# Performance work log

Hardware: AMD Instinct MI355X
Metric: run time of the kernel (lower is better)

Reference implementation:

```python
import jax, jax.numpy as jnp
import numpy as np

N_NODES = 100000
N_HEDGES = 200000
N_INC = 1000000
N_GRAPHS = 256
H = 64        # h_dim
HE = 35       # hedge_fea_dim
HOUT = 128    # hout_dim
NL = 3        # n_layers
EPS = 1e-5


def _segment_mean(vals, idx, num_segments):
    s = jax.ops.segment_sum(vals, idx, num_segments=num_segments)
    cnt = jax.ops.segment_sum(jnp.ones((vals.shape[0],), vals.dtype), idx,
                              num_segments=num_segments)
    return s / jnp.maximum(cnt, 1.0)[:, None]


def _bn(z, g, b):
    # training-mode BatchNorm1d: batch stats, biased variance
    m = jnp.mean(z, axis=0)
    v = jnp.var(z, axis=0)
    return (z - m) * jax.lax.rsqrt(v + EPS) * g + b


def setup_inputs() -> dict:
    key = jax.random.key(0)
    ks = jax.random.split(key, 32)
    inp = {
        "x": jax.random.normal(ks[0], (N_NODES, 92), jnp.float32),
        "node_idx": jax.random.randint(ks[1], (N_INC,), 0, N_NODES),
        "hedge_idx": jax.random.randint(ks[2], (N_INC,), 0, N_HEDGES),
        "hedge_attr": jax.random.normal(ks[3], (N_HEDGES, HE), jnp.float32),
        "batch": jnp.sort(jax.random.randint(ks[4], (N_NODES,), 0, N_GRAPHS)),
    }
    s = 0.05
    cat = H + HE  # 99
    inp["embed_w"] = jax.random.normal(ks[5], (92, H), jnp.float32) * s
    inp["embed_b"] = jnp.zeros((H,), jnp.float32)
    inp["f1_w"] = jax.random.normal(ks[6], (NL, cat, HE), jnp.float32) * s
    inp["f1_b"] = jnp.zeros((NL, HE), jnp.float32)
    inp["c1_w"] = jax.random.normal(ks[7], (NL, cat, HE), jnp.float32) * s
    inp["c1_b"] = jnp.zeros((NL, HE), jnp.float32)
    inp["f2_w"] = jax.random.normal(ks[8], (NL, cat, H), jnp.float32) * s
    inp["f2_b"] = jnp.zeros((NL, H), jnp.float32)
    inp["c2_w"] = jax.random.normal(ks[9], (NL, cat, H), jnp.float32) * s
    inp["c2_b"] = jnp.zeros((NL, H), jnp.float32)
    inp["bnf_g"] = jnp.ones((NL, HE), jnp.float32)
    inp["bnf_b"] = jnp.zeros((NL, HE), jnp.float32)
    inp["bnc_g"] = jnp.ones((NL, HE), jnp.float32)
    inp["bnc_b"] = jnp.zeros((NL, HE), jnp.float32)
    inp["bno_g"] = jnp.ones((NL, H), jnp.float32)
    inp["bno_b"] = jnp.zeros((NL, H), jnp.float32)
    inp["l2_w"] = jax.random.normal(ks[10], (H, HOUT), jnp.float32) * s
    inp["l2_b"] = jnp.zeros((HOUT,), jnp.float32)
    inp["out_w"] = jax.random.normal(ks[11], (HOUT, 1), jnp.float32) * s
    inp["out_b"] = jnp.zeros((1,), jnp.float32)
    return inp


def reference(x, node_idx, hedge_idx, hedge_attr, batch,
              embed_w, embed_b, f1_w, f1_b, c1_w, c1_b,
              f2_w, f2_b, c2_w, c2_b,
              bnf_g, bnf_b, bnc_g, bnc_b, bno_g, bno_b,
              l2_w, l2_b, out_w, out_b):
    sp = jax.nn.softplus
    x = x @ embed_w + embed_b  # [N, H]
    for i in range(NL):
        # gather node feats per incidence, mean over each hyperedge
        hx = _segment_mean(x[node_idx], hedge_idx, N_HEDGES)       # [NH, H]
        msg = jnp.concatenate([hx, hedge_attr], axis=1)            # [NH, H+HE]
        z_f = _bn(msg @ f1_w[i] + f1_b[i], bnf_g[i], bnf_b[i])
        z_c = _bn(msg @ c1_w[i] + c1_b[i], bnc_g[i], bnc_b[i])
        hedge_attr = jax.nn.sigmoid(z_f) * sp(z_c)                 # [NH, HE]
        z = jnp.concatenate([x[node_idx], hedge_attr[hedge_idx]], axis=-1)  # [E, H+HE]
        o = jax.nn.sigmoid(z @ f2_w[i] + f2_b[i]) * sp(z @ c2_w[i] + c2_b[i])  # [E, H]
        o = _segment_mean(o, node_idx, N_NODES)                    # [N, H]
        o = _bn(o, bno_g[i], bno_b[i])
        x = sp(o + x)
    pooled = _segment_mean(x, batch, N_GRAPHS)                     # [G, H]
    h = sp(pooled @ l2_w + l2_b)                                   # [G, HOUT]
    return h @ out_w + out_b                                       # [G, 1]
```

## Files before the change

kernel.cpp:

```cpp
#include <hip/hip_runtime.h>
#include <math.h>

#define N_NODES 100000
#define N_HEDGES 200000
#define N_INC 1000000
#define N_GRAPHS 256
#define HD 64
#define HE 35
#define CAT 99
#define EPSB 1e-5f

typedef __attribute__((ext_vector_type(8))) short short8;
typedef __attribute__((ext_vector_type(4))) float f32x4;

__device__ __forceinline__ float sp_f(float x) {
  return fmaxf(x, 0.f) + __logf(1.f + __expf(-fabsf(x)));
}
__device__ __forceinline__ float sig_f(float x) {
  return __builtin_amdgcn_rcpf(1.f + __expf(-x));
}
__device__ __forceinline__ unsigned bfr(float x) {
  unsigned u = __float_as_uint(x);
  return (u + 0x7fffu + ((u >> 16) & 1u)) >> 16;
}
__device__ __forceinline__ unsigned pk2(float lo, float hi) {
  return bfr(lo) | (bfr(hi) << 16);
}
__device__ __forceinline__ float blo(unsigned v) { return __uint_as_float(v << 16); }
__device__ __forceinline__ float bhi(unsigned v) {
  return __uint_as_float(v & 0xffff0000u);
}
__device__ __forceinline__ float bf2f(unsigned short s) {
  return __uint_as_float(((unsigned)s) << 16);
}

__global__ __launch_bounds__(256) void k_hist(const int* __restrict__ nidx,
                                              const int* __restrict__ hidx,
                                              int* __restrict__ degN,
                                              int* __restrict__ degH,
                                              int* __restrict__ rankN,
                                              int* __restrict__ rankH) {
  int e = blockIdx.x * 256 + threadIdx.x;
  if (e >= N_INC) return;
  rankH[e] = atomicAdd(&degH[hidx[e]], 1);
  rankN[e] = atomicAdd(&degN[nidx[e]], 1);
}

#define CHB ((N_HEDGES + 255) / 256)
#define CNB ((N_NODES + 255) / 256)

__global__ __launch_bounds__(256) void k_bsum(const int* __restrict__ degH,
                                              const int* __restrict__ degN,
                                              int* __restrict__ bsum) {
  __shared__ int s[256];
  int b = blockIdx.x, t = threadIdx.x;
  const int* deg;
  int n, i;
  if (b < CHB) {
    deg = degH; n = N_HEDGES; i = b * 256 + t;
  } else {
    deg = degN; n = N_NODES; i = (b - CHB) * 256 + t;
  }
  s[t] = (i < n) ? deg[i] : 0;
  __syncthreads();
  for (int st = 128; st > 0; st >>= 1) {
    if (t < st) s[t] += s[t + st];
    __syncthreads();
  }
  if (t == 0) bsum[b] = s[0];
}

__global__ __launch_bounds__(64) void k_bscan(int* __restrict__ bsum) {
  int seg0 = (blockIdx.x == 0) ? 0 : CHB;
  int segn = (blockIdx.x == 0) ? CHB : CNB;
  int lane = threadIdx.x;
  int carry = 0;
  for (int base = 0; base < segn; base += 64) {
    int i = base + lane;
    int orig = (i < segn) ? bsum[seg0 + i] : 0;
    int v = orig;
    for (int st = 1; st < 64; st <<= 1) {
      int u = __shfl_up(v, st);
      if (lane >= st) v += u;
    }
    int total = __shfl(v, 63);
    if (i < segn) bsum[seg0 + i] = carry + (v - orig);
    carry += total;
  }
}

__global__ __launch_bounds__(256) void k_alloc2(const int* __restrict__ degH,
                                                const int* __restrict__ degN,
                                                const int* __restrict__ bsum,
                                                int* __restrict__ offH,
                                                int* __restrict__ offN,
                                                float* __restrict__ invdH) {
  __shared__ int s[256];
  int b = blockIdx.x, t = threadIdx.x;
  const int* deg;
  int* off;
  int n, i;
  bool isH = (b < CHB);
  if (isH) {
    deg = degH; off = offH; n = N_HEDGES; i = b * 256 + t;
  } else {
    deg = degN; off = offN; n = N_NODES; i = (b - CHB) * 256 + t;
  }
  int d = (i < n) ? deg[i] : 0;
  s[t] = d;
  __syncthreads();
  for (int st = 1; st < 256; st <<= 1) {
    int u = 0;
    if (t >= st) u = s[t - st];
    __syncthreads();
    if (t >= st) s[t] += u;
    __syncthreads();
  }
  if (i < n) {
    off[i] = s[t] - d + bsum[b];
    if (isH) invdH[i] = 1.f / (float)max(d, 1);
  }
}

__global__ __launch_bounds__(256) void k_fill(const int* __restrict__ nidx,
                                              const int* __restrict__ hidx,
                                              const int* __restrict__ rankH,
                                              const int* __restrict__ rankN,
                                              const int* __restrict__ offH,
                                              const int* __restrict__ offN,
                                              int* __restrict__ permHn,
                                              int* __restrict__ permNh) {
  int e = blockIdx.x * 256 + threadIdx.x;
  if (e >= N_INC) return;
  int nd = nidx[e], hg = hidx[e];
  permHn[offH[hg] + rankH[e]] = nd;
  permNh[offN[nd] + rankN[e]] = hg;
}

__global__ __launch_bounds__(64) void k_wpack(const float* __restrict__ f1w,
                                              const float* __restrict__ c1w,
                                              uint4* __restrict__ wpk) {
  int b = blockIdx.x;
  int layer = b / 20, rem = b % 20, ct = rem / 4, ks = rem % 4;
  int lane = threadIdx.x;
  int col = ct * 16 + (lane & 15);
  int k0 = ks * 32 + (lane >> 4) * 8;
  const float* wf = f1w + layer * CAT * HE;
  const float* wc = c1w + layer * CAT * HE;
  unsigned v[4];
#pragma unroll
  for (int p = 0; p < 4; ++p) {
    float lo = 0.f, hi = 0.f;
    int ka = k0 + p * 2, kb = ka + 1;
    if (ka < 99) {
      if (col < 35) lo = wf[ka * 35 + col];
      else if (col >= 36 && col < 71) lo = wc[ka * 35 + (col - 36)];
    }
    if (kb < 99) {
      if (col < 35) hi = wf[kb * 35 + col];
      else if (col >= 36 && col < 71) hi = wc[kb * 35 + (col - 36)];
    }
    v[p] = pk2(lo, hi);
  }
  uint4 o;
  o.x = v[0]; o.y = v[1]; o.z = v[2]; o.w = v[3];
  wpk[b * 64 + lane] = o;
}

__global__ __launch_bounds__(256) void k_cvt_ha(const float* __restrict__ src,
                                                unsigned short* __restrict__ dst,
                                                int n) {
  int t = blockIdx.x * 256 + threadIdx.x;
  if (t < n) dst[t] = (unsigned short)bfr(src[t]);
}

__global__ __launch_bounds__(256) void k_embed(const float* __restrict__ x,
                                               const float* __restrict__ w,
                                               const float* __restrict__ b,
                                               unsigned short* __restrict__ outb) {
  __shared__ float ws[92 * 64];
  __shared__ float rs[16][93];
  int tid = threadIdx.x;
  for (int i = tid; i < 92 * 64; i += 256) ws[i] = w[i];
  int r0 = blockIdx.x * 16;
  for (int i = tid; i < 16 * 92; i += 256) {
    int r = i / 92, k = i - r * 92;
    rs[r][k] = x[(r0 + r) * 92 + k];
  }
  __syncthreads();
  int h = tid & 63;
  float bias = b[h];
  for (int rr = tid >> 6; rr < 16; rr += 4) {
    float acc = bias;
    for (int k = 0; k < 92; ++k) acc += rs[rr][k] * ws[k * 64 + h];
    outb[(r0 + rr) * 64 + h] = (unsigned short)bfr(acc);
  }
}

#define GR 64
__global__ __launch_bounds__(256) void k_hedge_gemm(
    const unsigned short* __restrict__ xb, const int* __restrict__ permHn,
    const int* __restrict__ offH, const int* __restrict__ degH,
    const float* __restrict__ invdH, const unsigned short* __restrict__ hab,
    const uint4* __restrict__ wpk, unsigned short* __restrict__ z,
    float* __restrict__ stats) {
  __shared__ unsigned short msg[GR * 128];
  __shared__ float ps[160];
  int tid = threadIdx.x;
  int w = tid >> 6, lane = tid & 63;
  int r0 = blockIdx.x * GR;
  if (tid < 160) ps[tid] = 0.f;

  short8 bfg[5][4];
#pragma unroll
  for (int ct = 0; ct < 5; ++ct)
#pragma unroll
    for (int ks = 0; ks < 4; ++ks)
      bfg[ct][ks] = __builtin_bit_cast(short8, wpk[(ct * 4 + ks) * 64 + lane]);

  char* mb = (char*)msg;
  for (int r = 0; r < 16; ++r) {
    int rloc = w * 16 + r;
    int row = r0 + rloc;
    float acc = 0.f;
    unsigned short hv = 0, mv = 0;
    if (row < N_HEDGES) {
      int o = offH[row], d = degH[row];
      int k = 0;
      for (; k + 4 <= d; k += 4) {
        int n0 = permHn[o + k], n1 = permHn[o + k + 1];
        int n2 = permHn[o + k + 2], n3 = permHn[o + k + 3];
        acc += (bf2f(xb[(size_t)n0 * 64 + lane]) + bf2f(xb[(size_t)n1 * 64 + lane])) +
               (bf2f(xb[(size_t)n2 * 64 + lane]) + bf2f(xb[(size_t)n3 * 64 + lane]));
      }
      for (; k < d; ++k) acc += bf2f(xb[(size_t)permHn[o + k] * 64 + lane]);
      mv = (unsigned short)bfr(acc * invdH[row]);
      if (lane < 35) hv = hab[(size_t)row * 35 + lane];
    }
    int swz = (rloc & 7) << 4;
    *(unsigned short*)(mb + ((rloc * 256 + lane * 2) ^ swz)) = mv;
    *(unsigned short*)(mb + ((rloc * 256 + 128 + lane * 2) ^ swz)) = hv;
  }
  __syncthreads();

  {
    int rloc = w * 16 + (lane & 15);
    short8 a[4];
#pragma unroll
    for (int ks = 0; ks < 4; ++ks) {
      int byte = rloc * 256 + (ks * 32 + (lane >> 4) * 8) * 2;
      a[ks] = *(const short8*)(mb + (byte ^ ((rloc & 7) << 4)));
    }
#pragma unroll
    for (int ct = 0; ct < 5; ++ct) {
      f32x4 acc = {0.f, 0.f, 0.f, 0.f};
#pragma unroll
      for (int ks = 0; ks < 4; ++ks)
        acc = __builtin_amdgcn_mfma_f32_16x16x32_bf16(a[ks], bfg[ct][ks], acc, 0, 0, 0);
      float s = (acc[0] + acc[1]) + (acc[2] + acc[3]);
      float q = (acc[0] * acc[0] + acc[1] * acc[1]) +
                (acc[2] * acc[2] + acc[3] * acc[3]);
      s += __shfl_xor(s, 16);
      s += __shfl_xor(s, 32);
      q += __shfl_xor(q, 16);
      q += __shfl_xor(q, 32);
      int col = ct * 16 + (lane & 15);
      if ((lane >> 4) == 0 && col < 72) {
        atomicAdd(&ps[col], s);
        atomicAdd(&ps[80 + col], q);
      }
      int growb = r0 + w * 16 + ((lane >> 4) << 2);
      if (col < 72) {
#pragma unroll
        for (int r = 0; r < 4; ++r) {
          int grow = growb + r;
          if (grow < N_HEDGES)
            z[(size_t)grow * 72 + col] = (unsigned short)bfr(acc[r]);
        }
      }
    }
  }
  __syncthreads();
  if (tid < 160) atomicAdd(&stats[tid], ps[tid]);
}

__global__ __launch_bounds__(256) void k_hedge_apply(
    const unsigned short* __restrict__ z, const float* __restrict__ stats,
    const float* __restrict__ gf, const float* __restrict__ bf_,
    const float* __restrict__ gc, const float* __restrict__ bc_,
    unsigned short* __restrict__ hab) {
  int t = blockIdx.x * 256 + threadIdx.x;
  if (t >= N_HEDGES * 35) return;
  int r = t / 35, c = t - r * 35;
  const float inv = 1.f / N_HEDGES;
  float mf = stats[c] * inv;
  float vf = stats[80 + c] * inv - mf * mf;
  float mc = stats[36 + c] * inv;
  float vc = stats[116 + c] * inv - mc * mc;
  const unsigned short* zr = &z[(size_t)r * 72];
  float nf = (bf2f(zr[c]) - mf) * rsqrtf(vf + EPSB) * gf[c] + bf_[c];
  float nc = (bf2f(zr[36 + c]) - mc) * rsqrtf(vc + EPSB) * gc[c] + bc_[c];
  hab[t] = (unsigned short)bfr(sig_f(nf) * sp_f(nc));
}

__global__ __launch_bounds__(256) void k_uv_node(const unsigned short* __restrict__ xb,
                                                 const float* __restrict__ f2w,
                                                 const float* __restrict__ c2w,
                                                 unsigned* __restrict__ Ufc) {
  __shared__ float wf[64 * 64];
  __shared__ float wc[64 * 64];
  __shared__ float rs[16][65];
  int tid = threadIdx.x;
  for (int i = tid; i < 64 * 64; i += 256) {
    wf[i] = f2w[i];
    wc[i] = c2w[i];
  }
  int r0 = blockIdx.x * 16;
  for (int i = tid; i < 16 * 64; i += 256) {
    int r = i >> 6, k = i & 63;
    rs[r][k] = bf2f(xb[(size_t)(r0 + r) * 64 + k]);
  }
  __syncthreads();
  int h = tid & 63, rb = tid >> 6;
  float af0 = 0, af1 = 0, af2 = 0, af3 = 0, ac0 = 0, ac1 = 0, ac2 = 0, ac3 = 0;
  for (int k = 0; k < 64; ++k) {
    float wfv = wf[k * 64 + h], wcv = wc[k * 64 + h];
    float m0 = rs[rb][k], m1 = rs[rb + 4][k], m2 = rs[rb + 8][k], m3 = rs[rb + 12][k];
    af0 += m0 * wfv; ac0 += m0 * wcv;
    af1 += m1 * wfv; ac1 += m1 * wcv;
    af2 += m2 * wfv; ac2 += m2 * wcv;
    af3 += m3 * wfv; ac3 += m3 * wcv;
  }
  int row = r0 + rb;
  Ufc[row * 64 + h] = pk2(af0, ac0);
  Ufc[(row + 4) * 64 + h] = pk2(af1, ac1);
  Ufc[(row + 8) * 64 + h] = pk2(af2, ac2);
  Ufc[(row + 12) * 64 + h] = pk2(af3, ac3);
}

__global__ __launch_bounds__(256) void k_uv_hedge(
    const unsigned short* __restrict__ hab, const float* __restrict__ f2wb,
    const float* __restrict__ c2wb, const float* __restrict__ f2b,
    const float* __restrict__ c2b, unsigned* __restrict__ Vfc) {
  __shared__ float wf[35 * 64];
  __shared__ float wc[35 * 64];
  __shared__ float rs[16][36];
  int tid = threadIdx.x;
  for (int i = tid; i < 35 * 64; i += 256) {
    wf[i] = f2wb[i];
    wc[i] = c2wb[i];
  }
  int r0 = blockIdx.x * 16;
  for (int i = tid; i < 16 * 35; i += 256) {
    int r = i / 35, k = i - r * 35;
    rs[r][k] = bf2f(hab[(r0 + r) * 35 + k]);
  }
  __syncthreads();
  int h = tid & 63, rb = tid >> 6;
  float af0, af1, af2, af3, ac0, ac1, ac2, ac3;
  af0 = af1 = af2 = af3 = f2b[h];
  ac0 = ac1 = ac2 = ac3 = c2b[h];
  for (int k = 0; k < 35; ++k) {
    float wfv = wf[k * 64 + h], wcv = wc[k * 64 + h];
    float m0 = rs[rb][k], m1 = rs[rb + 4][k], m2 = rs[rb + 8][k], m3 = rs[rb + 12][k];
    af0 += m0 * wfv; ac0 += m0 * wcv;
    af1 += m1 * wfv; ac1 += m1 * wcv;
    af2 += m2 * wfv; ac2 += m2 * wcv;
    af3 += m3 * wfv; ac3 += m3 * wcv;
  }
  int row = r0 + rb;
  Vfc[row * 64 + h] = pk2(af0, ac0);
  Vfc[(row + 4) * 64 + h] = pk2(af1, ac1);
  Vfc[(row + 8) * 64 + h] = pk2(af2, ac2);
  Vfc[(row + 12) * 64 + h] = pk2(af3, ac3);
}

__device__ __forceinline__ float act2(float uf, float uc, unsigned v) {
  float a = uf + blo(v);
  float b = uc + bhi(v);
  return sig_f(a) * sp_f(b);
}
__global__ __launch_bounds__(256) void k_node_aggr(const int* __restrict__ permNh,
                                                   const int* __restrict__ offN,
                                                   const int* __restrict__ degN,
                                                   const unsigned* __restrict__ Ufc,
                                                   const unsigned* __restrict__ Vfc,
                                                   float* __restrict__ o) {
  int gt = blockIdx.x * 256 + threadIdx.x;
  int wid = gt >> 6, h = gt & 63;
  if (wid >= N_NODES) return;
  int off = offN[wid], d = degN[wid];
  unsigned u = Ufc[wid * 64 + h];
  float uf = blo(u), uc = bhi(u);
  float acc = 0.f;
  int k = 0;
  for (; k + 4 <= d; k += 4) {
    int h0 = permNh[off + k], h1 = permNh[off + k + 1];
    int h2 = permNh[off + k + 2], h3 = permNh[off + k + 3];
    unsigned v0 = Vfc[h0 * 64 + h];
    unsigned v1 = Vfc[h1 * 64 + h];
    unsigned v2 = Vfc[h2 * 64 + h];
    unsigned v3 = Vfc[h3 * 64 + h];
    acc += (act2(uf, uc, v0) + act2(uf, uc, v1)) +
           (act2(uf, uc, v2) + act2(uf, uc, v3));
  }
  for (; k < d; ++k) acc += act2(uf, uc, Vfc[permNh[off + k] * 64 + h]);
  o[wid * 64 + h] = acc / (float)max(d, 1);
}

__global__ __launch_bounds__(256) void k_ostats(const float* __restrict__ o,
                                                float* __restrict__ stats) {
  int h = threadIdx.x & 63;
  int rs = threadIdx.x >> 6;
  float s = 0.f, sq = 0.f;
  for (int r = blockIdx.x * 4 + rs; r < N_NODES; r += gridDim.x * 4) {
    float v = o[r * 64 + h];
    s += v;
    sq += v * v;
  }
  __shared__ float ls[4][2][64];
  ls[rs][0][h] = s;
  ls[rs][1][h] = sq;
  __syncthreads();
  if (threadIdx.x < 64) {
    float ts = ls[0][0][h] + ls[1][0][h] + ls[2][0][h] + ls[3][0][h];
    float tq = ls[0][1][h] + ls[1][1][h] + ls[2][1][h] + ls[3][1][h];
    atomicAdd(&stats[h], ts);
    atomicAdd(&stats[64 + h], tq);
  }
}

__global__ __launch_bounds__(256) void k_update(unsigned short* __restrict__ xb,
                                                const float* __restrict__ o,
                                                const float* __restrict__ stats,
                                                const float* __restrict__ g,
                                                const float* __restrict__ b) {
  int t = blockIdx.x * 256 + threadIdx.x;
  int h = t & 63;
  float mean = stats[h] * (1.f / N_NODES);
  float var = stats[64 + h] * (1.f / N_NODES) - mean * mean;
  float is = rsqrtf(var + EPSB);
  float v = (o[t] - mean) * is * g[h] + b[h];
  float r = sp_f(v + bf2f(xb[t]));
  xb[t] = (unsigned short)bfr(r);
}

#define PR 512
__global__ __launch_bounds__(256) void k_pool(const unsigned short* __restrict__ xb,
                                              const int* __restrict__ batch,
                                              float* __restrict__ pooled,
                                              float* __restrict__ gcnt) {
  int h = threadIdx.x & 63, rs = threadIdx.x >> 6;
  int r0 = blockIdx.x * PR;
  int rend = min(r0 + PR, N_NODES);
  int gcur = -1;
  float acc = 0.f;
  int cnt = 0;
  for (int r = r0 + rs; r < rend; r += 4) {
    int g = batch[r];
    if (g != gcur) {
      if (gcur >= 0) {
        atomicAdd(&pooled[gcur * 64 + h], acc);
        if (h == 0) atomicAdd(&gcnt[gcur], (float)cnt);
      }
      gcur = g;
      acc = 0.f;
      cnt = 0;
    }
    acc += bf2f(xb[(size_t)r * 64 + h]);
    cnt++;
  }
  if (gcur >= 0) {
    atomicAdd(&pooled[gcur * 64 + h], acc);
    if (h == 0) atomicAdd(&gcnt[gcur], (float)cnt);
  }
}

__global__ __launch_bounds__(128) void k_final(const float* __restrict__ pooled,
                                               const float* __restrict__ gcnt,
                                               const float* __restrict__ l2w,
                                               const float* __restrict__ l2b,
                                               const float* __restrict__ ow,
                                               const float* __restrict__ ob,
                                               float* __restrict__ out) {
  int g = blockIdx.x;
  int t = threadIdx.x;
  __shared__ float row[64];
  __shared__ float hh[128];
  if (t < 64) row[t] = pooled[g * 64 + t] / fmaxf(gcnt[g], 1.f);
  __syncthreads();
  float acc = l2b[t];
  for (int k = 0; k < 64; ++k) acc += row[k] * l2w[k * 128 + t];
  hh[t] = sp_f(acc) * ow[t];
  __syncthreads();
  for (int s = 64; s > 0; s >>= 1) {
    if (t < s) hh[t] += hh[t + s];
    __syncthreads();
  }
  if (t == 0) out[g] = hh[0] + ob[0];
}

extern "C" void kernel_launch(void* const* d_in, const int* in_sizes, int n_in,
                              void* d_out, int out_size, void* d_ws, size_t ws_size,
                              hipStream_t stream) {
  const float* x_in = (const float*)d_in[0];
  const int* node_idx = (const int*)d_in[1];
  const int* hedge_idx = (const int*)d_in[2];
  const float* hedge_attr = (const float*)d_in[3];
  const int* batch = (const int*)d_in[4];
  const float* embed_w = (const float*)d_in[5];
  const float* embed_b = (const float*)d_in[6];
  const float* f1_w = (const float*)d_in[7];
  const float* c1_w = (const float*)d_in[9];
  const float* f2_w = (const float*)d_in[11];
  const float* f2_b = (const float*)d_in[12];
  const float* c2_w = (const float*)d_in[13];
  const float* c2_b = (const float*)d_in[14];
  const float* bnf_g = (const float*)d_in[15];
  const float* bnf_b = (const float*)d_in[16];
  const float* bnc_g = (const float*)d_in[17];
  const float* bnc_b = (const float*)d_in[18];
  const float* bno_g = (const float*)d_in[19];
  const float* bno_b = (const float*)d_in[20];
  const float* l2_w = (const float*)d_in[21];
  const float* l2_b = (const float*)d_in[22];
  const float* out_w = (const float*)d_in[23];
  const float* out_b = (const float*)d_in[24];

  char* base = (char*)d_ws;
  size_t off = 0;
  auto alloc = [&](size_t bytes) {
    size_t o = off;
    off = (off + bytes + 255) & ~(size_t)255;
    return o;
  };
  unsigned short* xbf = (unsigned short*)(base + alloc((size_t)N_NODES * 64 * 2));
  unsigned short* hab = (unsigned short*)(base + alloc((size_t)N_HEDGES * 35 * 2));
  unsigned* Vfc = (unsigned*)(base + alloc((size_t)N_HEDGES * 64 * 4));
  float* obuf = (float*)(base + alloc((size_t)N_NODES * 64 * 4));
  unsigned short* zbuf = (unsigned short*)Vfc;
  unsigned* Ufc = (unsigned*)(base + alloc((size_t)N_NODES * 64 * 4));
  uint4* wpk = (uint4*)(base + alloc((size_t)60 * 64 * 16));
  float* hstatsA = (float*)(base + alloc(3 * 160 * 4));
  float* ostatsA = (float*)(base + alloc(3 * 128 * 4));
  float* pooled = (float*)(base + alloc((size_t)N_GRAPHS * 64 * 4));
  float* gcnt = (float*)(base + alloc((size_t)N_GRAPHS * 4));
  int* degH = (int*)(base + alloc((size_t)N_HEDGES * 4));
  int* degN = (int*)(base + alloc((size_t)N_NODES * 4));
  int* offH = (int*)(base + alloc((size_t)N_HEDGES * 4));
  int* offN = (int*)(base + alloc((size_t)N_NODES * 4));
  float* invdH = (float*)(base + alloc((size_t)N_HEDGES * 4));
  int* bsum = (int*)(base + alloc((size_t)(CHB + CNB) * 4));
  int* rankH = (int*)(base + alloc((size_t)N_INC * 4));
  int* rankN = (int*)(base + alloc((size_t)N_INC * 4));
  int* permHn = (int*)(base + alloc((size_t)N_INC * 4));
  int* permNh = (int*)(base + alloc((size_t)N_INC * 4));
  (void)ws_size;
  (void)in_sizes;
  (void)n_in;
  (void)out_size;

  hipMemsetAsync(degH, 0,
                 (size_t)((char*)degN - (char*)degH) + (size_t)N_NODES * 4, stream);
  k_hist<<<(N_INC + 255) / 256, 256, 0, stream>>>(node_idx, hedge_idx, degN, degH,
                                                  rankN, rankH);
  k_bsum<<<CHB + CNB, 256, 0, stream>>>(degH, degN, bsum);
  k_bscan<<<2, 64, 0, stream>>>(bsum);
  k_alloc2<<<CHB + CNB, 256, 0, stream>>>(degH, degN, bsum, offH, offN, invdH);
  k_fill<<<(N_INC + 255) / 256, 256, 0, stream>>>(node_idx, hedge_idx, rankH, rankN,
                                                  offH, offN, permHn, permNh);
  k_wpack<<<60, 64, 0, stream>>>(f1_w, c1_w, wpk);
  k_cvt_ha<<<(N_HEDGES * 35 + 255) / 256, 256, 0, stream>>>(hedge_attr, hab,
                                                            N_HEDGES * 35);
  k_embed<<<N_NODES / 16, 256, 0, stream>>>(x_in, embed_w, embed_b, xbf);

  hipMemsetAsync(hstatsA, 0, (size_t)((char*)ostatsA - (char*)hstatsA) + 3 * 128 * 4,
                 stream);

  for (int i = 0; i < 3; ++i) {
    float* hstats = hstatsA + i * 160;
    float* ostats = ostatsA + i * 128;

    k_hedge_gemm<<<(N_HEDGES + GR - 1) / GR, 256, 0, stream>>>(
        xbf, permHn, offH, degH, invdH, hab, wpk + (size_t)i * 20 * 64, zbuf, hstats);
    k_hedge_apply<<<(N_HEDGES * 35 + 255) / 256, 256, 0, stream>>>(
        zbuf, hstats, bnf_g + i * HE, bnf_b + i * HE, bnc_g + i * HE, bnc_b + i * HE,
        hab);

    k_uv_node<<<N_NODES / 16, 256, 0, stream>>>(xbf, f2_w + i * CAT * 64,
                                                c2_w + i * CAT * 64, Ufc);
    k_uv_hedge<<<N_HEDGES / 16, 256, 0, stream>>>(
        hab, f2_w + i * CAT * 64 + 64 * 64, c2_w + i * CAT * 64 + 64 * 64,
        f2_b + i * 64, c2_b + i * 64, Vfc);

    k_node_aggr<<<N_NODES * 64 / 256, 256, 0, stream>>>(permNh, offN, degN, Ufc, Vfc,
                                                        obuf);

    k_ostats<<<1024, 256, 0, stream>>>(obuf, ostats);
    k_update<<<N_NODES * 64 / 256, 256, 0, stream>>>(xbf, obuf, ostats,
                                                     bno_g + i * 64, bno_b + i * 64);
  }

  hipMemsetAsync(pooled, 0, (size_t)((char*)gcnt - (char*)pooled) + N_GRAPHS * 4,
                 stream);
  k_pool<<<(N_NODES + PR - 1) / PR, 256, 0, stream>>>(xbf, batch, pooled, gcnt);
  k_final<<<N_GRAPHS, 128, 0, stream>>>(pooled, gcnt, l2_w, l2_b, out_w, out_b,
                                        (float*)d_out);
}
```

Baseline: 1.407 ms.

## Fuse hedge BN-apply with V projection, fuse node stats, flatten hedge gather

```diff
diff --git a/kernel.cpp b/kernel.cpp
--- a/kernel.cpp
+++ b/kernel.cpp
@@ -129,9 +129,11 @@
                                               const int* __restrict__ offH,
                                               const int* __restrict__ offN,
                                               int* __restrict__ permHn,
-                                              int* __restrict__ permNh) {
+                                              int* __restrict__ permNh,
+                                              int* __restrict__ offH_sent) {
   int e = blockIdx.x * 256 + threadIdx.x;
   if (e >= N_INC) return;
+  if (e == 0) *offH_sent = N_INC;
   int nd = nidx[e], hg = hidx[e];
   permHn[offH[hg] + rankH[e]] = nd;
   permNh[offN[nd] + rankN[e]] = hg;
@@ -200,12 +202,12 @@
 #define GR 64
 __global__ __launch_bounds__(256) void k_hedge_gemm(
     const unsigned short* __restrict__ xb, const int* __restrict__ permHn,
-    const int* __restrict__ offH, const int* __restrict__ degH,
-    const float* __restrict__ invdH, const unsigned short* __restrict__ hab,
-    const uint4* __restrict__ wpk, unsigned short* __restrict__ z,
-    float* __restrict__ stats) {
+    const int* __restrict__ offH, const float* __restrict__ invdH,
+    const unsigned short* __restrict__ hab, const uint4* __restrict__ wpk,
+    unsigned short* __restrict__ z, float* __restrict__ stats) {
   __shared__ unsigned short msg[GR * 128];
   __shared__ float ps[160];
+  __shared__ int bndL[4][18];
   int tid = threadIdx.x;
   int w = tid >> 6, lane = tid & 63;
   int r0 = blockIdx.x * GR;
@@ -219,27 +221,47 @@
       bfg[ct][ks] = __builtin_bit_cast(short8, wpk[(ct * 4 + ks) * 64 + lane]);
 
   char* mb = (char*)msg;
-  for (int r = 0; r < 16; ++r) {
-    int rloc = w * 16 + r;
-    int row = r0 + rloc;
-    float acc = 0.f;
-    unsigned short hv = 0, mv = 0;
-    if (row < N_HEDGES) {
-      int o = offH[row], d = degH[row];
-      int k = 0;
-      for (; k + 4 <= d; k += 4) {
-        int n0 = permHn[o + k], n1 = permHn[o + k + 1];
-        int n2 = permHn[o + k + 2], n3 = permHn[o + k + 3];
-        acc += (bf2f(xb[(size_t)n0 * 64 + lane]) + bf2f(xb[(size_t)n1 * 64 + lane])) +
-               (bf2f(xb[(size_t)n2 * 64 + lane]) + bf2f(xb[(size_t)n3 * 64 + lane]));
+  for (int i = tid; i < GR * 64; i += 256) {
+    int r = i >> 6, c = 64 + (i & 63);
+    unsigned short hv = 0;
+    if (c < 99) hv = hab[(size_t)(r0 + r) * 35 + (c - 64)];
+    *(unsigned short*)(mb + ((r * 256 + c * 2) ^ ((r & 7) << 4))) = hv;
+  }
+
+  int r0w = r0 + w * 16;
+  if (lane < 17) bndL[w][lane] = offH[r0w + lane];
+  int eBeg = bndL[w][0], eEnd = bndL[w][16];
+
+  int j = 0;
+  int nb = bndL[w][1];
+  float acc = 0.f;
+  for (int chunk = eBeg; chunk < eEnd; chunk += 8) {
+    float v[8];
+#pragma unroll
+    for (int t = 0; t < 8; ++t) {
+      int idx = permHn[min(chunk + t, eEnd - 1)];
+      v[t] = bf2f(xb[(size_t)idx * 64 + lane]);
+    }
+#pragma unroll
+    for (int t = 0; t < 8; ++t) {
+      int e = chunk + t;
+      if (e >= eEnd) break;
+      while (e >= nb) {
+        int rl = w * 16 + j;
+        unsigned short mv = (unsigned short)bfr(acc * invdH[r0w + j]);
+        *(unsigned short*)(mb + ((rl * 256 + lane * 2) ^ ((rl & 7) << 4))) = mv;
+        acc = 0.f;
+        ++j;
+        nb = bndL[w][j + 1];
       }
-      for (; k < d; ++k) acc += bf2f(xb[(size_t)permHn[o + k] * 64 + lane]);
-      mv = (unsigned short)bfr(acc * invdH[row]);
-      if (lane < 35) hv = hab[(size_t)row * 35 + lane];
-    }
-    int swz = (rloc & 7) << 4;
-    *(unsigned short*)(mb + ((rloc * 256 + lane * 2) ^ swz)) = mv;
-    *(unsigned short*)(mb + ((rloc * 256 + 128 + lane * 2) ^ swz)) = hv;
+      acc += v[t];
+    }
+  }
+  for (; j < 16; ++j) {
+    int rl = w * 16 + j;
+    unsigned short mv = (unsigned short)bfr(acc * invdH[r0w + j]);
+    *(unsigned short*)(mb + ((rl * 256 + lane * 2) ^ ((rl & 7) << 4))) = mv;
+    acc = 0.f;
   }
   __syncthreads();
 
@@ -253,13 +275,13 @@
     }
 #pragma unroll
     for (int ct = 0; ct < 5; ++ct) {
-      f32x4 acc = {0.f, 0.f, 0.f, 0.f};
+      f32x4 acc4 = {0.f, 0.f, 0.f, 0.f};
 #pragma unroll
       for (int ks = 0; ks < 4; ++ks)
-        acc = __builtin_amdgcn_mfma_f32_16x16x32_bf16(a[ks], bfg[ct][ks], acc, 0, 0, 0);
-      float s = (acc[0] + acc[1]) + (acc[2] + acc[3]);
-      float q = (acc[0] * acc[0] + acc[1] * acc[1]) +
-                (acc[2] * acc[2] + acc[3] * acc[3]);
+        acc4 = __builtin_amdgcn_mfma_f32_16x16x32_bf16(a[ks], bfg[ct][ks], acc4, 0, 0, 0);
+      float s = (acc4[0] + acc4[1]) + (acc4[2] + acc4[3]);
+      float q = (acc4[0] * acc4[0] + acc4[1] * acc4[1]) +
+                (acc4[2] * acc4[2] + acc4[3] * acc4[3]);
       s += __shfl_xor(s, 16);
       s += __shfl_xor(s, 32);
       q += __shfl_xor(q, 16);
@@ -272,11 +294,8 @@
       int growb = r0 + w * 16 + ((lane >> 4) << 2);
       if (col < 72) {
 #pragma unroll
-        for (int r = 0; r < 4; ++r) {
-          int grow = growb + r;
-          if (grow < N_HEDGES)
-            z[(size_t)grow * 72 + col] = (unsigned short)bfr(acc[r]);
-        }
+        for (int r = 0; r < 4; ++r)
+          z[(size_t)(growb + r) * 72 + col] = (unsigned short)bfr(acc4[r]);
       }
     }
   }
@@ -284,23 +303,64 @@
   if (tid < 160) atomicAdd(&stats[tid], ps[tid]);
 }
 
-__global__ __launch_bounds__(256) void k_hedge_apply(
+__global__ __launch_bounds__(256) void k_hedge_post(
     const unsigned short* __restrict__ z, const float* __restrict__ stats,
     const float* __restrict__ gf, const float* __restrict__ bf_,
     const float* __restrict__ gc, const float* __restrict__ bc_,
-    unsigned short* __restrict__ hab) {
-  int t = blockIdx.x * 256 + threadIdx.x;
-  if (t >= N_HEDGES * 35) return;
-  int r = t / 35, c = t - r * 35;
-  const float inv = 1.f / N_HEDGES;
-  float mf = stats[c] * inv;
-  float vf = stats[80 + c] * inv - mf * mf;
-  float mc = stats[36 + c] * inv;
-  float vc = stats[116 + c] * inv - mc * mc;
-  const unsigned short* zr = &z[(size_t)r * 72];
-  float nf = (bf2f(zr[c]) - mf) * rsqrtf(vf + EPSB) * gf[c] + bf_[c];
-  float nc = (bf2f(zr[36 + c]) - mc) * rsqrtf(vc + EPSB) * gc[c] + bc_[c];
-  hab[t] = (unsigned short)bfr(sig_f(nf) * sp_f(nc));
+    const float* __restrict__ f2wb, const float* __restrict__ c2wb,
+    const float* __restrict__ f2b, const float* __restrict__ c2b,
+    unsigned short* __restrict__ hab, unsigned* __restrict__ Vfc) {
+  __shared__ float wf[35 * 64];
+  __shared__ float wc[35 * 64];
+  __shared__ float rs[16][36];
+  __shared__ float sf[4][35];
+  int tid = threadIdx.x;
+  for (int i = tid; i < 35 * 64; i += 256) {
+    wf[i] = f2wb[i];
+    wc[i] = c2wb[i];
+  }
+  if (tid < 35) {
+    const float inv = 1.f / N_HEDGES;
+    float mf = stats[tid] * inv;
+    float vf = stats[80 + tid] * inv - mf * mf;
+    float mc = stats[36 + tid] * inv;
+    float vc = stats[116 + tid] * inv - mc * mc;
+    float a = rsqrtf(vf + EPSB) * gf[tid];
+    float b = rsqrtf(vc + EPSB) * gc[tid];
+    sf[0][tid] = a;
+    sf[1][tid] = bf_[tid] - mf * a;
+    sf[2][tid] = b;
+    sf[3][tid] = bc_[tid] - mc * b;
+  }
+  __syncthreads();
+  int r0 = blockIdx.x * 16;
+  for (int i = tid; i < 16 * 35; i += 256) {
+    int r = i / 35, c = i - r * 35;
+    const unsigned short* zr = &z[(size_t)(r0 + r) * 72];
+    float nf = bf2f(zr[c]) * sf[0][c] + sf[1][c];
+    float nc = bf2f(zr[36 + c]) * sf[2][c] + sf[3][c];
+    float ha = sig_f(nf) * sp_f(nc);
+    rs[r][c] = ha;
+    hab[(size_t)(r0 + r) * 35 + c] = (unsigned short)bfr(ha);
+  }
+  __syncthreads();
+  int h = tid & 63, rb = tid >> 6;
+  float af0, af1, af2, af3, ac0, ac1, ac2, ac3;
+  af0 = af1 = af2 = af3 = f2b[h];
+  ac0 = ac1 = ac2 = ac3 = c2b[h];
+  for (int k = 0; k < 35; ++k) {
+    float wfv = wf[k * 64 + h], wcv = wc[k * 64 + h];
+    float m0 = rs[rb][k], m1 = rs[rb + 4][k], m2 = rs[rb + 8][k], m3 = rs[rb + 12][k];
+    af0 += m0 * wfv; ac0 += m0 * wcv;
+    af1 += m1 * wfv; ac1 += m1 * wcv;
+    af2 += m2 * wfv; ac2 += m2 * wcv;
+    af3 += m3 * wfv; ac3 += m3 * wcv;
+  }
+  int row = r0 + rb;
+  Vfc[row * 64 + h] = pk2(af0, ac0);
+  Vfc[(row + 4) * 64 + h] = pk2(af1, ac1);
+  Vfc[(row + 8) * 64 + h] = pk2(af2, ac2);
+  Vfc[(row + 12) * 64 + h] = pk2(af3, ac3);
 }
 
 __global__ __launch_bounds__(256) void k_uv_node(const unsigned short* __restrict__ xb,
@@ -338,95 +398,55 @@
   Ufc[(row + 12) * 64 + h] = pk2(af3, ac3);
 }
 
-__global__ __launch_bounds__(256) void k_uv_hedge(
-    const unsigned short* __restrict__ hab, const float* __restrict__ f2wb,
-    const float* __restrict__ c2wb, const float* __restrict__ f2b,
-    const float* __restrict__ c2b, unsigned* __restrict__ Vfc) {
-  __shared__ float wf[35 * 64];
-  __shared__ float wc[35 * 64];
-  __shared__ float rs[16][36];
-  int tid = threadIdx.x;
-  for (int i = tid; i < 35 * 64; i += 256) {
-    wf[i] = f2wb[i];
-    wc[i] = c2wb[i];
-  }
-  int r0 = blockIdx.x * 16;
-  for (int i = tid; i < 16 * 35; i += 256) {
-    int r = i / 35, k = i - r * 35;
-    rs[r][k] = bf2f(hab[(r0 + r) * 35 + k]);
-  }
-  __syncthreads();
-  int h = tid & 63, rb = tid >> 6;
-  float af0, af1, af2, af3, ac0, ac1, ac2, ac3;
-  af0 = af1 = af2 = af3 = f2b[h];
-  ac0 = ac1 = ac2 = ac3 = c2b[h];
-  for (int k = 0; k < 35; ++k) {
-    float wfv = wf[k * 64 + h], wcv = wc[k * 64 + h];
-    float m0 = rs[rb][k], m1 = rs[rb + 4][k], m2 = rs[rb + 8][k], m3 = rs[rb + 12][k];
-    af0 += m0 * wfv; ac0 += m0 * wcv;
-    af1 += m1 * wfv; ac1 += m1 * wcv;
-    af2 += m2 * wfv; ac2 += m2 * wcv;
-    af3 += m3 * wfv; ac3 += m3 * wcv;
-  }
-  int row = r0 + rb;
-  Vfc[row * 64 + h] = pk2(af0, ac0);
-  Vfc[(row + 4) * 64 + h] = pk2(af1, ac1);
-  Vfc[(row + 8) * 64 + h] = pk2(af2, ac2);
-  Vfc[(row + 12) * 64 + h] = pk2(af3, ac3);
-}
-
 __device__ __forceinline__ float act2(float uf, float uc, unsigned v) {
   float a = uf + blo(v);
   float b = uc + bhi(v);
   return sig_f(a) * sp_f(b);
 }
+#define NAGG_GRID 2048
 __global__ __launch_bounds__(256) void k_node_aggr(const int* __restrict__ permNh,
                                                    const int* __restrict__ offN,
                                                    const int* __restrict__ degN,
                                                    const unsigned* __restrict__ Ufc,
                                                    const unsigned* __restrict__ Vfc,
-                                                   float* __restrict__ o) {
-  int gt = blockIdx.x * 256 + threadIdx.x;
-  int wid = gt >> 6, h = gt & 63;
-  if (wid >= N_NODES) return;
-  int off = offN[wid], d = degN[wid];
-  unsigned u = Ufc[wid * 64 + h];
-  float uf = blo(u), uc = bhi(u);
-  float acc = 0.f;
-  int k = 0;
-  for (; k + 4 <= d; k += 4) {
-    int h0 = permNh[off + k], h1 = permNh[off + k + 1];
-    int h2 = permNh[off + k + 2], h3 = permNh[off + k + 3];
-    unsigned v0 = Vfc[h0 * 64 + h];
-    unsigned v1 = Vfc[h1 * 64 + h];
-    unsigned v2 = Vfc[h2 * 64 + h];
-    unsigned v3 = Vfc[h3 * 64 + h];
-    acc += (act2(uf, uc, v0) + act2(uf, uc, v1)) +
-           (act2(uf, uc, v2) + act2(uf, uc, v3));
-  }
-  for (; k < d; ++k) acc += act2(uf, uc, Vfc[permNh[off + k] * 64 + h]);
-  o[wid * 64 + h] = acc / (float)max(d, 1);
-}
-
-__global__ __launch_bounds__(256) void k_ostats(const float* __restrict__ o,
-                                                float* __restrict__ stats) {
-  int h = threadIdx.x & 63;
-  int rs = threadIdx.x >> 6;
-  float s = 0.f, sq = 0.f;
-  for (int r = blockIdx.x * 4 + rs; r < N_NODES; r += gridDim.x * 4) {
-    float v = o[r * 64 + h];
-    s += v;
-    sq += v * v;
-  }
-  __shared__ float ls[4][2][64];
-  ls[rs][0][h] = s;
-  ls[rs][1][h] = sq;
-  __syncthreads();
-  if (threadIdx.x < 64) {
-    float ts = ls[0][0][h] + ls[1][0][h] + ls[2][0][h] + ls[3][0][h];
-    float tq = ls[0][1][h] + ls[1][1][h] + ls[2][1][h] + ls[3][1][h];
-    atomicAdd(&stats[h], ts);
-    atomicAdd(&stats[64 + h], tq);
+                                                   float* __restrict__ o,
+                                                   float* __restrict__ stats) {
+  int tid = threadIdx.x;
+  int h = tid & 63, sub = tid >> 6;
+  float sacc = 0.f, qacc = 0.f;
+  for (int grp = blockIdx.x; grp < N_NODES / 4; grp += NAGG_GRID) {
+    int wid = grp * 4 + sub;
+    int off = offN[wid], d = degN[wid];
+    unsigned u = Ufc[wid * 64 + h];
+    float uf = blo(u), uc = bhi(u);
+    float acc = 0.f;
+    int k = 0;
+    for (; k + 4 <= d; k += 4) {
+      int h0 = permNh[off + k], h1 = permNh[off + k + 1];
+      int h2 = permNh[off + k + 2], h3 = permNh[off + k + 3];
+      unsigned v0 = Vfc[h0 * 64 + h];
+      unsigned v1 = Vfc[h1 * 64 + h];
+      unsigned v2 = Vfc[h2 * 64 + h];
+      unsigned v3 = Vfc[h3 * 64 + h];
+      acc += (act2(uf, uc, v0) + act2(uf, uc, v1)) +
+             (act2(uf, uc, v2) + act2(uf, uc, v3));
+    }
+    for (; k < d; ++k) acc += act2(uf, uc, Vfc[permNh[off + k] * 64 + h]);
+    float val = acc / (float)max(d, 1);
+    o[(size_t)wid * 64 + h] = val;
+    sacc += val;
+    qacc += val * val;
+  }
+  __shared__ float ls[2][4][64];
+  ls[0][sub][h] = sacc;
+  ls[1][sub][h] = qacc;
+  __syncthreads();
+  if (tid < 64) {
+    atomicAdd(&stats[h], ls[0][0][h] + ls[0][1][h] + ls[0][2][h] + ls[0][3][h]);
+  } else if (tid < 128) {
+    int hh = tid - 64;
+    atomicAdd(&stats[64 + hh],
+              ls[1][0][hh] + ls[1][1][hh] + ls[1][2][hh] + ls[1][3][hh]);
   }
 }
 
@@ -537,8 +557,8 @@
   unsigned short* xbf = (unsigned short*)(base + alloc((size_t)N_NODES * 64 * 2));
   unsigned short* hab = (unsigned short*)(base + alloc((size_t)N_HEDGES * 35 * 2));
   unsigned* Vfc = (unsigned*)(base + alloc((size_t)N_HEDGES * 64 * 4));
+  unsigned short* zbuf = (unsigned short*)(base + alloc((size_t)N_HEDGES * 72 * 2));
   float* obuf = (float*)(base + alloc((size_t)N_NODES * 64 * 4));
-  unsigned short* zbuf = (unsigned short*)Vfc;
   unsigned* Ufc = (unsigned*)(base + alloc((size_t)N_NODES * 64 * 4));
   uint4* wpk = (uint4*)(base + alloc((size_t)60 * 64 * 16));
   float* hstatsA = (float*)(base + alloc(3 * 160 * 4));
@@ -547,7 +567,7 @@
   float* gcnt = (float*)(base + alloc((size_t)N_GRAPHS * 4));
   int* degH = (int*)(base + alloc((size_t)N_HEDGES * 4));
   int* degN = (int*)(base + alloc((size_t)N_NODES * 4));
-  int* offH = (int*)(base + alloc((size_t)N_HEDGES * 4));
+  int* offH = (int*)(base + alloc((size_t)(N_HEDGES + 1) * 4));
   int* offN = (int*)(base + alloc((size_t)N_NODES * 4));
   float* invdH = (float*)(base + alloc((size_t)N_HEDGES * 4));
   int* bsum = (int*)(base + alloc((size_t)(CHB + CNB) * 4));
@@ -568,7 +588,8 @@
   k_bscan<<<2, 64, 0, stream>>>(bsum);
   k_alloc2<<<CHB + CNB, 256, 0, stream>>>(degH, degN, bsum, offH, offN, invdH);
   k_fill<<<(N_INC + 255) / 256, 256, 0, stream>>>(node_idx, hedge_idx, rankH, rankN,
-                                                  offH, offN, permHn, permNh);
+                                                  offH, offN, permHn, permNh,
+                                                  &offH[N_HEDGES]);
   k_wpack<<<60, 64, 0, stream>>>(f1_w, c1_w, wpk);
   k_cvt_ha<<<(N_HEDGES * 35 + 255) / 256, 256, 0, stream>>>(hedge_attr, hab,
                                                             N_HEDGES * 35);
@@ -581,22 +602,19 @@
     float* hstats = hstatsA + i * 160;
     float* ostats = ostatsA + i * 128;
 
-    k_hedge_gemm<<<(N_HEDGES + GR - 1) / GR, 256, 0, stream>>>(
-        xbf, permHn, offH, degH, invdH, hab, wpk + (size_t)i * 20 * 64, zbuf, hstats);
-    k_hedge_apply<<<(N_HEDGES * 35 + 255) / 256, 256, 0, stream>>>(
+    k_hedge_gemm<<<N_HEDGES / GR, 256, 0, stream>>>(
+        xbf, permHn, offH, invdH, hab, wpk + (size_t)i * 20 * 64, zbuf, hstats);
+    k_hedge_post<<<N_HEDGES / 16, 256, 0, stream>>>(
         zbuf, hstats, bnf_g + i * HE, bnf_b + i * HE, bnc_g + i * HE, bnc_b + i * HE,
-        hab);
+        f2_w + i * CAT * 64 + 64 * 64, c2_w + i * CAT * 64 + 64 * 64,
+        f2_b + i * 64, c2_b + i * 64, hab, Vfc);
 
     k_uv_node<<<N_NODES / 16, 256, 0, stream>>>(xbf, f2_w + i * CAT * 64,
                                                 c2_w + i * CAT * 64, Ufc);
-    k_uv_hedge<<<N_HEDGES / 16, 256, 0, stream>>>(
-        hab, f2_w + i * CAT * 64 + 64 * 64, c2_w + i * CAT * 64 + 64 * 64,
-        f2_b + i * 64, c2_b + i * 64, Vfc);
-
-    k_node_aggr<<<N_NODES * 64 / 256, 256, 0, stream>>>(permNh, offN, degN, Ufc, Vfc,
-                                                        obuf);
-
-    k_ostats<<<1024, 256, 0, stream>>>(obuf, ostats);
+
+    k_node_aggr<<<NAGG_GRID, 256, 0, stream>>>(permNh, offN, degN, Ufc, Vfc, obuf,
+                                               ostats);
+
     k_update<<<N_NODES * 64 / 256, 256, 0, stream>>>(xbf, obuf, ostats,
                                                      bno_g + i * 64, bno_b + i * 64);
   }
```

Result: faster. 1.270 ms (-9.8%).
